# Kernel optimization log

Measured on AMD Instinct MI355X. Metric: run time of the kernel, lower is better.

Reference implementation:

```python
import jax, jax.numpy as jnp
import numpy as np

IN_FEATURES = 1024
FEATURES = 1024
GRID_SIZE = 5
SPLINE_ORDER = 3
GRID_MIN, GRID_MAX = -2.0, 2.0
EPS = 1e-7


def setup_inputs() -> dict:
    key = jax.random.key(0)
    k_x, k_w, k_ss, k_bs = jax.random.split(key, 4)
    x = jax.random.normal(k_x, (4096, IN_FEATURES), dtype=jnp.float32)
    # Extended knot sequence: grid_size + 2*spline_order + 1 knots
    h = (GRID_MAX - GRID_MIN) / GRID_SIZE
    grid = GRID_MIN + h * jnp.arange(-SPLINE_ORDER, GRID_SIZE + SPLINE_ORDER + 1,
                                     dtype=jnp.float32)  # (12,)
    K = GRID_SIZE + SPLINE_ORDER  # number of B-spline basis functions = 8
    # glorot_uniform over (I, O, K)
    limit = float(np.sqrt(6.0 / (IN_FEATURES + FEATURES)))
    spline_weight = jax.random.uniform(k_w, (IN_FEATURES, FEATURES, K),
                                       minval=-limit, maxval=limit, dtype=jnp.float32)
    spline_scaler = jax.random.uniform(k_ss, (IN_FEATURES, FEATURES),
                                       minval=-limit, maxval=limit, dtype=jnp.float32)
    base_scaler = jax.random.uniform(k_bs, (IN_FEATURES, FEATURES),
                                     minval=-limit, maxval=limit, dtype=jnp.float32)
    return {"x": x, "grid": grid, "spline_weight": spline_weight,
            "spline_scaler": spline_scaler, "base_scaler": base_scaler}


def _bspline_bases(x, grid):
    # x: (B, I); grid: (G+2S+1,) -> bases: (B, I, G+S)
    xe = x[..., None]
    # order-0 indicator bases on each knot interval
    bases = ((xe >= grid[:-1]) & (xe < grid[1:])).astype(x.dtype)
    for p in range(1, SPLINE_ORDER + 1):  # Cox-de Boor recursion
        left = (xe - grid[:-(p + 1)]) / (grid[p:-1] - grid[:-(p + 1)] + EPS)
        right = (grid[p + 1:] - xe) / (grid[p + 1:] - grid[1:-p] + EPS)
        bases = left * bases[..., :-1] + right * bases[..., 1:]
    return bases


def reference(x, grid, spline_weight, spline_scaler, base_scaler):
    # Base path: b(x) = swish(x) = x * sigmoid(x), summed over inputs with base_scaler
    base_out = jnp.einsum('bi,io->bo', x * jax.nn.sigmoid(x), base_scaler)
    # Spline path: per-connection spline with per-connection scaling
    bases = _bspline_bases(x, grid)                       # (B, I, K)
    scaled_w = spline_weight * spline_scaler[..., None]   # (I, O, K)
    spline_out = jnp.einsum('bik,iok->bo', bases, scaled_w)
    return base_out + spline_out
```

## Files before the change

### kernel.cpp

```cpp
#include <hip/hip_runtime.h>
#include <hip/hip_bf16.h>
#include <cstdint>
#include <cstddef>

#define I_F   1024
#define O_F   1024
#define BATCH 4096
#define KDIM  9216
#define EPSC  1e-7f

typedef __bf16 bf16;
typedef __bf16 bf16x4 __attribute__((ext_vector_type(4)));
typedef __bf16 bf16x8 __attribute__((ext_vector_type(8)));
typedef float  f32x4  __attribute__((ext_vector_type(4)));
typedef float  f32x16 __attribute__((ext_vector_type(16)));

__global__ __launch_bounds__(256) void act_kernel(const float* __restrict__ x,
                                                  const float* __restrict__ grid,
                                                  bf16* __restrict__ A) {
    int t  = blockIdx.x * 256 + threadIdx.x;
    int b  = t >> 8;
    int i0 = (t & 255) << 2;
    f32x4 xv4 = *(const f32x4*)(x + (size_t)b * I_F + i0);

    float g[12];
#pragma unroll
    for (int j = 0; j < 12; ++j) g[j] = grid[j];
    float r1[11], r2[10], r3[9];
#pragma unroll
    for (int j = 0; j < 11; ++j) r1[j] = __builtin_amdgcn_rcpf(g[j + 1] - g[j] + EPSC);
#pragma unroll
    for (int j = 0; j < 10; ++j) r2[j] = __builtin_amdgcn_rcpf(g[j + 2] - g[j] + EPSC);
#pragma unroll
    for (int j = 0; j < 9;  ++j) r3[j] = __builtin_amdgcn_rcpf(g[j + 3] - g[j] + EPSC);

    float sw[4];
    float bs8[4][8];
#pragma unroll
    for (int e = 0; e < 4; ++e) {
        float xv = xv4[e];
        float bas[11];
#pragma unroll
        for (int j = 0; j < 11; ++j)
            bas[j] = (xv >= g[j] && xv < g[j + 1]) ? 1.0f : 0.0f;
#pragma unroll
        for (int j = 0; j < 10; ++j)
            bas[j] = (xv - g[j]) * r1[j] * bas[j] + (g[j + 2] - xv) * r1[j + 1] * bas[j + 1];
#pragma unroll
        for (int j = 0; j < 9; ++j)
            bas[j] = (xv - g[j]) * r2[j] * bas[j] + (g[j + 3] - xv) * r2[j + 1] * bas[j + 1];
#pragma unroll
        for (int j = 0; j < 8; ++j)
            bas[j] = (xv - g[j]) * r3[j] * bas[j] + (g[j + 4] - xv) * r3[j + 1] * bas[j + 1];
#pragma unroll
        for (int k = 0; k < 8; ++k) bs8[e][k] = bas[k];
        float sig = 1.0f / (1.0f + __expf(-xv));
        sw[e] = xv * sig;
    }

    bf16* outp = A + (size_t)b * KDIM + i0;
    *(bf16x4*)(outp) = (bf16x4){(bf16)sw[0], (bf16)sw[1], (bf16)sw[2], (bf16)sw[3]};
#pragma unroll
    for (int k = 0; k < 8; ++k)
        *(bf16x4*)(outp + (size_t)(k + 1) * 1024) =
            (bf16x4){(bf16)bs8[0][k], (bf16)bs8[1][k], (bf16)bs8[2][k], (bf16)bs8[3][k]};
}

__global__ __launch_bounds__(256) void wprep_kernel(const float* __restrict__ w,
                                                    const float* __restrict__ ss,
                                                    const float* __restrict__ bs,
                                                    bf16* __restrict__ Wt) {
    int g = blockIdx.x * 256 + threadIdx.x;
    int i  = g & 1023;
    int o0 = (g >> 10) << 3;
    size_t io0 = (size_t)i * 1024 + o0;
    f32x4 ssv0 = *(const f32x4*)(ss + io0);
    f32x4 ssv1 = *(const f32x4*)(ss + io0 + 4);
    f32x4 bsv0 = *(const f32x4*)(bs + io0);
    f32x4 bsv1 = *(const f32x4*)(bs + io0 + 4);
#pragma unroll
    for (int oo = 0; oo < 8; ++oo) {
        int o = o0 + oo;
        float scale = (oo < 4) ? ssv0[oo & 3] : ssv1[oo & 3];
        float base  = (oo < 4) ? bsv0[oo & 3] : bsv1[oo & 3];
        const float* wp = w + (io0 + oo) * 8;
        f32x4 w0 = *(const f32x4*)(wp);
        f32x4 w1 = *(const f32x4*)(wp + 4);

        bf16* outp = Wt + (size_t)o * KDIM + i;
        outp[0] = (bf16)base;
#pragma unroll
        for (int k = 0; k < 4; ++k) outp[(size_t)(k + 1) * 1024] = (bf16)(w0[k] * scale);
#pragma unroll
        for (int k = 0; k < 4; ++k) outp[(size_t)(k + 5) * 1024] = (bf16)(w1[k] * scale);
    }
}

__device__ __forceinline__ void load_lds16(const bf16* g, bf16* l) {
    __builtin_amdgcn_global_load_lds(
        (__attribute__((address_space(1))) void*)g,
        (__attribute__((address_space(3))) void*)l, 16, 0, 0);
}

__global__ __launch_bounds__(512, 2) void gemm_kernel(const bf16* __restrict__ A,
                                                      const bf16* __restrict__ Wt,
                                                      bf16* __restrict__ parts,
                                                      int split, int ktiles) {
    __shared__ __align__(16) bf16 SA[4][8192];
    __shared__ __align__(16) bf16 SB[4][8192];

    const int t    = threadIdx.x;
    const int lane = t & 63;
    const int w    = t >> 6;

    const int nwg8 = gridDim.x >> 3;
    const int L    = (blockIdx.x & 7) * nwg8 + (blockIdx.x >> 3);
    const int nper = split << 4;
    const int tn   = L / nper;
    const int rem  = L - tn * nper;
    const int s    = rem >> 4;
    const int tm   = rem & 15;

    const int row0 = tm << 8;
    const int col0 = tn << 8;
    const size_t k0 = (size_t)s * ktiles * 32;

    const int sr = lane >> 2;
    const int lc = (lane & 3) ^ ((lane >> 3) & 3);
    const bf16* gA0 = A  + (size_t)(row0 + w * 16 + sr) * KDIM + k0 + lc * 8;
    const bf16* gB0 = Wt + (size_t)(col0 + w * 16 + sr) * KDIM + k0 + lc * 8;

    const int wm  = w >> 2;
    const int wn  = w & 3;
    const int r31 = lane & 31;
    const int hi  = lane >> 5;
    const int swb = (r31 >> 1) & 3;

    f32x16 acc[4][2];
#pragma unroll
    for (int mt = 0; mt < 4; ++mt)
#pragma unroll
        for (int nt = 0; nt < 2; ++nt)
#pragma unroll
            for (int r = 0; r < 16; ++r) acc[mt][nt][r] = 0.f;

    auto stage = [&](int j) {
        const int sl = j & 3;
        const bf16* pa = gA0 + (size_t)j * 32;
        const bf16* pb = gB0 + (size_t)j * 32;
        load_lds16(pa,                      &SA[sl][w * 512]);
        load_lds16(pa + (size_t)128 * KDIM, &SA[sl][4096 + w * 512]);
        load_lds16(pb,                      &SB[sl][w * 512]);
        load_lds16(pb + (size_t)128 * KDIM, &SB[sl][4096 + w * 512]);
    };

    auto frag_load_ks = [&](int sl, int ks, bf16x8 (&af)[4], bf16x8 (&bv)[2]) {
        const int cp = ((ks * 2 + hi) ^ swb) << 3;
        af[0] = *(const bf16x8*)&SA[sl][(wm * 128 +  0 + r31) * 32 + cp];
        bv[0] = *(const bf16x8*)&SB[sl][(wn * 64  +  0 + r31) * 32 + cp];
        af[1] = *(const bf16x8*)&SA[sl][(wm * 128 + 32 + r31) * 32 + cp];
        bv[1] = *(const bf16x8*)&SB[sl][(wn * 64  + 32 + r31) * 32 + cp];
        af[2] = *(const bf16x8*)&SA[sl][(wm * 128 + 64 + r31) * 32 + cp];
        af[3] = *(const bf16x8*)&SA[sl][(wm * 128 + 96 + r31) * 32 + cp];
    };

    auto do_mfma = [&](bf16x8 (&af0)[4], bf16x8 (&bv0)[2],
                       bf16x8 (&af1)[4], bf16x8 (&bv1)[2]) {
        __builtin_amdgcn_s_setprio(1);
#pragma unroll
        for (int mt = 0; mt < 4; ++mt)
#pragma unroll
            for (int nt = 0; nt < 2; ++nt)
                acc[mt][nt] = __builtin_amdgcn_mfma_f32_32x32x16_bf16(
                    af0[mt], bv0[nt], acc[mt][nt], 0, 0, 0);
#pragma unroll
        for (int mt = 0; mt < 4; ++mt)
#pragma unroll
            for (int nt = 0; nt < 2; ++nt)
                acc[mt][nt] = __builtin_amdgcn_mfma_f32_32x32x16_bf16(
                    af1[mt], bv1[nt], acc[mt][nt], 0, 0, 0);
        __builtin_amdgcn_s_setprio(0);
    };

    stage(0); stage(1); stage(2);

    int j = 0;
    for (; j < ktiles - 3; ++j) {
        asm volatile("s_waitcnt vmcnt(8)" ::: "memory");
        __builtin_amdgcn_s_barrier();
        asm volatile("" ::: "memory");
        bf16x8 af0[4], bv0[2], af1[4], bv1[2];
        frag_load_ks(j & 3, 0, af0, bv0);
        frag_load_ks(j & 3, 1, af1, bv1);
        stage(j + 3);
        do_mfma(af0, bv0, af1, bv1);
    }
    {
        asm volatile("s_waitcnt vmcnt(8)" ::: "memory");
        __builtin_amdgcn_s_barrier();
        asm volatile("" ::: "memory");
        bf16x8 af0[4], bv0[2], af1[4], bv1[2];
        frag_load_ks(j & 3, 0, af0, bv0);
        frag_load_ks(j & 3, 1, af1, bv1);
        do_mfma(af0, bv0, af1, bv1);
        ++j;
    }
    {
        asm volatile("s_waitcnt vmcnt(4)" ::: "memory");
        __builtin_amdgcn_s_barrier();
        asm volatile("" ::: "memory");
        bf16x8 af0[4], bv0[2], af1[4], bv1[2];
        frag_load_ks(j & 3, 0, af0, bv0);
        frag_load_ks(j & 3, 1, af1, bv1);
        do_mfma(af0, bv0, af1, bv1);
        ++j;
    }
    {
        asm volatile("s_waitcnt vmcnt(0)" ::: "memory");
        __builtin_amdgcn_s_barrier();
        asm volatile("" ::: "memory");
        bf16x8 af0[4], bv0[2], af1[4], bv1[2];
        frag_load_ks(j & 3, 0, af0, bv0);
        frag_load_ks(j & 3, 1, af1, bv1);
        do_mfma(af0, bv0, af1, bv1);
    }

    bf16* cp = parts + (size_t)s * BATCH * O_F
             + (size_t)(row0 + wm * 128) * O_F + col0 + wn * 64 + r31;
#pragma unroll
    for (int mt = 0; mt < 4; ++mt)
#pragma unroll
        for (int nt = 0; nt < 2; ++nt)
#pragma unroll
            for (int r = 0; r < 16; ++r) {
                int rl = (r & 3) + 8 * (r >> 2) + 4 * hi;
                cp[(size_t)(mt * 32 + rl) * O_F + nt * 32] = (bf16)acc[mt][nt][r];
            }
}

__global__ __launch_bounds__(256) void add_kernel(float* __restrict__ out,
                                                  const bf16* __restrict__ parts,
                                                  int np) {
    int t = blockIdx.x * 256 + threadIdx.x;
    f32x4 a = {0.f, 0.f, 0.f, 0.f};
    for (int p = 0; p < np; ++p) {
        bf16x4 b = *((const bf16x4*)(parts + (size_t)p * BATCH * O_F) + t);
#pragma unroll
        for (int e = 0; e < 4; ++e) a[e] += (float)b[e];
    }
    *((f32x4*)out + t) = a;
}

extern "C" void kernel_launch(void* const* d_in, const int* in_sizes, int n_in,
                              void* d_out, int out_size, void* d_ws, size_t ws_size,
                              hipStream_t stream) {
    const float* x    = (const float*)d_in[0];
    const float* grid = (const float*)d_in[1];
    const float* w    = (const float*)d_in[2];
    const float* ss   = (const float*)d_in[3];
    const float* bs   = (const float*)d_in[4];
    float* out = (float*)d_out;

    const size_t nA = (size_t)BATCH * KDIM * 2;
    const size_t nW = (size_t)O_F   * KDIM * 2;
    const size_t nP = (size_t)BATCH * O_F  * 2;

    bf16* A  = (bf16*)d_ws;
    bf16* Wt = (bf16*)((char*)d_ws + nA);
    bf16* parts = (bf16*)((char*)d_ws + nA + nW);

    act_kernel<<<(BATCH * I_F / 4) / 256, 256, 0, stream>>>(x, grid, A);
    wprep_kernel<<<(I_F * O_F / 8) / 256, 256, 0, stream>>>(w, ss, bs, Wt);

    int split = (ws_size >= nA + nW + 4 * nP) ? 4
              : (ws_size >= nA + nW + 2 * nP) ? 2 : 1;
    gemm_kernel<<<64 * split, 512, 0, stream>>>(A, Wt, parts, split, 288 / split);
    add_kernel<<<(BATCH * O_F / 4) / 256, 256, 0, stream>>>(out, parts, split);
}
```

Measured before the change: 126.6 us.

## Shrink GEMM tile to 256x128 with 4 waves and 3-stage LDS pipeline

Changes the GEMM workgroup from 512 threads with a 256x256 tile and 4-stage buffering to 256 threads with a 256x128 tile and 3-stage buffering. The grid becomes 512 blocks with split-K fixed at 4, and the XCD-aware block remapping becomes a simple modulo mapping. The aim is more workgroups for the 256 CUs, smaller LDS use and better occupancy. In exchange, B-tile reuse per workgroup drops, pipeline depth shrinks, and the workspace-size check for split is removed, so the kernel assumes enough workspace.

```diff
diff --git a/kernel.cpp b/kernel.cpp
--- a/kernel.cpp
+++ b/kernel.cpp
@@ -102,27 +102,24 @@
         (__attribute__((address_space(3))) void*)l, 16, 0, 0);
 }
 
-__global__ __launch_bounds__(512, 2) void gemm_kernel(const bf16* __restrict__ A,
+__global__ __launch_bounds__(256, 2) void gemm_kernel(const bf16* __restrict__ A,
                                                       const bf16* __restrict__ Wt,
                                                       bf16* __restrict__ parts,
                                                       int split, int ktiles) {
-    __shared__ __align__(16) bf16 SA[4][8192];
-    __shared__ __align__(16) bf16 SB[4][8192];
+    __shared__ __align__(16) bf16 SA[3][8192];
+    __shared__ __align__(16) bf16 SB[3][4096];
 
     const int t    = threadIdx.x;
     const int lane = t & 63;
     const int w    = t >> 6;
 
-    const int nwg8 = gridDim.x >> 3;
-    const int L    = (blockIdx.x & 7) * nwg8 + (blockIdx.x >> 3);
-    const int nper = split << 4;
-    const int tn   = L / nper;
-    const int rem  = L - tn * nper;
-    const int s    = rem >> 4;
-    const int tm   = rem & 15;
+    const int tn = blockIdx.x & 7;
+    const int i  = blockIdx.x >> 3;
+    const int s  = i >> 4;
+    const int tm = i & 15;
 
     const int row0 = tm << 8;
-    const int col0 = tn << 8;
+    const int col0 = tn << 7;
     const size_t k0 = (size_t)s * ktiles * 32;
 
     const int sr = lane >> 2;
@@ -130,8 +127,8 @@
     const bf16* gA0 = A  + (size_t)(row0 + w * 16 + sr) * KDIM + k0 + lc * 8;
     const bf16* gB0 = Wt + (size_t)(col0 + w * 16 + sr) * KDIM + k0 + lc * 8;
 
-    const int wm  = w >> 2;
-    const int wn  = w & 3;
+    const int wm  = w >> 1;
+    const int wn  = w & 1;
     const int r31 = lane & 31;
     const int hi  = lane >> 5;
     const int swb = (r31 >> 1) & 3;
@@ -145,13 +142,15 @@
             for (int r = 0; r < 16; ++r) acc[mt][nt][r] = 0.f;
 
     auto stage = [&](int j) {
-        const int sl = j & 3;
+        const int sl = j % 3;
         const bf16* pa = gA0 + (size_t)j * 32;
         const bf16* pb = gB0 + (size_t)j * 32;
-        load_lds16(pa,                      &SA[sl][w * 512]);
-        load_lds16(pa + (size_t)128 * KDIM, &SA[sl][4096 + w * 512]);
-        load_lds16(pb,                      &SB[sl][w * 512]);
-        load_lds16(pb + (size_t)128 * KDIM, &SB[sl][4096 + w * 512]);
+#pragma unroll
+        for (int q = 0; q < 4; ++q)
+            load_lds16(pa + (size_t)(q * 64) * KDIM, &SA[sl][(q * 64 + w * 16) * 32]);
+#pragma unroll
+        for (int q = 0; q < 2; ++q)
+            load_lds16(pb + (size_t)(q * 64) * KDIM, &SB[sl][(q * 64 + w * 16) * 32]);
     };
 
     auto frag_load_ks = [&](int sl, int ks, bf16x8 (&af)[4], bf16x8 (&bv)[2]) {
@@ -182,36 +181,26 @@
         __builtin_amdgcn_s_setprio(0);
     };
 
-    stage(0); stage(1); stage(2);
+    stage(0); stage(1);
 
     int j = 0;
-    for (; j < ktiles - 3; ++j) {
-        asm volatile("s_waitcnt vmcnt(8)" ::: "memory");
+    for (; j < ktiles - 2; ++j) {
+        asm volatile("s_waitcnt vmcnt(6)" ::: "memory");
         __builtin_amdgcn_s_barrier();
         asm volatile("" ::: "memory");
         bf16x8 af0[4], bv0[2], af1[4], bv1[2];
-        frag_load_ks(j & 3, 0, af0, bv0);
-        frag_load_ks(j & 3, 1, af1, bv1);
-        stage(j + 3);
+        frag_load_ks(j % 3, 0, af0, bv0);
+        frag_load_ks(j % 3, 1, af1, bv1);
+        stage(j + 2);
         do_mfma(af0, bv0, af1, bv1);
     }
     {
-        asm volatile("s_waitcnt vmcnt(8)" ::: "memory");
+        asm volatile("s_waitcnt vmcnt(6)" ::: "memory");
         __builtin_amdgcn_s_barrier();
         asm volatile("" ::: "memory");
         bf16x8 af0[4], bv0[2], af1[4], bv1[2];
-        frag_load_ks(j & 3, 0, af0, bv0);
-        frag_load_ks(j & 3, 1, af1, bv1);
-        do_mfma(af0, bv0, af1, bv1);
-        ++j;
-    }
-    {
-        asm volatile("s_waitcnt vmcnt(4)" ::: "memory");
-        __builtin_amdgcn_s_barrier();
-        asm volatile("" ::: "memory");
-        bf16x8 af0[4], bv0[2], af1[4], bv1[2];
-        frag_load_ks(j & 3, 0, af0, bv0);
-        frag_load_ks(j & 3, 1, af1, bv1);
+        frag_load_ks(j % 3, 0, af0, bv0);
+        frag_load_ks(j % 3, 1, af1, bv1);
         do_mfma(af0, bv0, af1, bv1);
         ++j;
     }
@@ -220,8 +209,8 @@
         __builtin_amdgcn_s_barrier();
         asm volatile("" ::: "memory");
         bf16x8 af0[4], bv0[2], af1[4], bv1[2];
-        frag_load_ks(j & 3, 0, af0, bv0);
-        frag_load_ks(j & 3, 1, af1, bv1);
+        frag_load_ks(j % 3, 0, af0, bv0);
+        frag_load_ks(j % 3, 1, af1, bv1);
         do_mfma(af0, bv0, af1, bv1);
     }
 
@@ -272,8 +261,6 @@
     act_kernel<<<(BATCH * I_F / 4) / 256, 256, 0, stream>>>(x, grid, A);
     wprep_kernel<<<(I_F * O_F / 8) / 256, 256, 0, stream>>>(w, ss, bs, Wt);
 
-    int split = (ws_size >= nA + nW + 4 * nP) ? 4
-              : (ws_size >= nA + nW + 2 * nP) ? 2 : 1;
-    gemm_kernel<<<64 * split, 512, 0, stream>>>(A, Wt, parts, split, 288 / split);
-    add_kernel<<<(BATCH * O_F / 4) / 256, 256, 0, stream>>>(out, parts, split);
-}
+    gemm_kernel<<<512, 256, 0, stream>>>(A, Wt, parts, 4, 72);
+    add_kernel<<<(BATCH * O_F / 4) / 256, 256, 0, stream>>>(out, parts, 4);
+}
```

After: 149.0 us. 17.7% more time.
